# Performance work log

Hardware: AMD Instinct MI355X
Metric: run time of the kernel (lower is better)

Reference implementation:

```python
import jax, jax.numpy as jnp
import numpy as np
import math

B, Z, H, HID, T = 16384, 128, 512, 512, 32
MIN_BETA = 0.1


def setup_inputs() -> dict:
    key = jax.random.key(0)
    ks = jax.random.split(key, 8)
    # cosine beta schedule, matching torch init: (1-min)*cos(pi*(1-t)*0.5)**2 + min, t in linspace(1,0,T)
    ts = np.linspace(1.0, 0.0, T)
    beta = ((1.0 - MIN_BETA) * np.cos(math.pi * (1.0 - ts) * 0.5) ** 2 + MIN_BETA).astype(np.float32)
    s = 1.0 / np.sqrt(Z + H)
    return {
        "context_embedding": jax.random.normal(ks[0], (B, H), jnp.float32),
        "eps0": jax.random.normal(ks[1], (B, Z), jnp.float32),
        "eps": jax.random.normal(ks[2], (T, B, Z), jnp.float32),
        "beta_schedule": jnp.asarray(beta),
        "sigma0": jnp.ones((1,), jnp.float32),
        "W1": jax.random.normal(ks[3], (Z + H, HID), jnp.float32) * s,
        "b1": jnp.zeros((HID,), jnp.float32),
        "W2": jax.random.normal(ks[4], (HID, Z), jnp.float32) * (1.0 / np.sqrt(HID)),
        "b2": jnp.zeros((Z,), jnp.float32),
        "t_emb": jax.random.normal(ks[5], (T, HID), jnp.float32) * 0.02,
        "target_mu": jax.random.normal(ks[6], (B, Z), jnp.float32),
    }


def _normal_log_prob(x, mu, sigma):
    # elementwise Normal(mu, sigma).log_prob(x)
    half_log_2pi = 0.5 * jnp.log(2.0 * jnp.pi)
    return -0.5 * jnp.square((x - mu) / sigma) - jnp.log(sigma) - half_log_2pi


def reference(context_embedding, eps0, eps, beta_schedule, sigma0, W1, b1, W2, b2, t_emb, target_mu):
    num_steps = beta_schedule.shape[0]
    delta_t = 1.0 / num_steps
    sig0 = sigma0[0]

    # prior sample z_0 ~ N(0, sigma0)
    z0 = sig0 * eps0  # [B, Z]

    # backward kernel at loop index i uses beta_schedule[i-1]; i=0 wraps to beta_schedule[-1]
    beta_bwd = jnp.roll(beta_schedule, 1)

    def control(z, te):
        hid = jax.nn.relu(jnp.concatenate([z, context_embedding], axis=-1) @ W1 + b1 + te)
        return hid @ W2 + b2  # [B, Z]

    def step(carry, xs):
        z_prev, log_w = carry
        beta_f, beta_b, eps_t, te = xs
        u = control(z_prev, te)
        # forward kernel
        mu_f = z_prev + (beta_f * z_prev + u) * delta_t
        sig_f = jnp.sqrt(2.0 * beta_f * delta_t) * sig0
        z_next = mu_f + sig_f * eps_t  # rsample
        # backward kernel (evaluated at z_next)
        mu_b = z_next - beta_b * z_next * delta_t
        sig_b = jnp.sqrt(2.0 * beta_b * delta_t) * sig0
        log_w = log_w + _normal_log_prob(z_prev, mu_b, sig_b) - _normal_log_prob(z_next, mu_f, sig_f)
        return (z_next, log_w), None

    init = (z0, jnp.zeros_like(z0))
    (z_T, log_w), _ = jax.lax.scan(step, init, (beta_schedule, beta_bwd, eps, t_emb))

    # terminal + prior correction: p_z_T = N(target_mu, 1), p_z_0 = N(0, sigma0)
    log_w = log_w + _normal_log_prob(z_T, target_mu, 1.0) - _normal_log_prob(z0, 0.0, sig0)
    return jnp.sum(jnp.mean(log_w, axis=0))
```

## Files before the change

kernel.cpp:

```cpp
#include <hip/hip_runtime.h>
#include <hip/hip_bf16.h>

#define NB 16384
#define NZ 128
#define NH 512
#define NHID 512
#define NT 32

typedef __attribute__((ext_vector_type(8))) short short8;
typedef __attribute__((ext_vector_type(4))) short short4v;
typedef __attribute__((ext_vector_type(4))) float f32x4;

__device__ __forceinline__ short f2bf(float x) {
    union { __hip_bfloat16 h; short s; } u; u.h = __float2bfloat16(x); return u.s;
}
__device__ __forceinline__ float bf2f(short s) {
    union { unsigned int u; float f; } v; v.u = ((unsigned int)(unsigned short)s) << 16; return v.f;
}

__global__ __launch_bounds__(64) void pack_weights(const float* __restrict__ W1,
                                                   const float* __restrict__ W2,
                                                   short* __restrict__ w1aT,
                                                   long* __restrict__ w2T8,
                                                   short* __restrict__ w1bT) {
    int f = blockIdx.x;
    int l = threadIdx.x;
    int quad = l >> 4, m = l & 15;
    if (f < 128) {
        int ht = f >> 2, kt = f & 3;
        short8 o;
#pragma unroll
        for (int j = 0; j < 8; ++j)
            o[j] = f2bf(W1[(size_t)(kt * 32 + quad * 8 + j) * NH + ht * 16 + m]);
        *(short8*)(w1aT + ((size_t)f * 64 + l) * 8) = o;
    } else if (f < 256) {
        int g = f - 128; int kt2 = g >> 3, jt = g & 7;
        float v[8];
#pragma unroll
        for (int j = 0; j < 8; ++j)
            v[j] = W2[(size_t)(kt2 * 32 + quad * 8 + j) * NZ + jt * 16 + m];
        int lo = __builtin_amdgcn_cvt_pk_fp8_f32(v[0], v[1], 0, false);
        lo = __builtin_amdgcn_cvt_pk_fp8_f32(v[2], v[3], lo, true);
        int hi = __builtin_amdgcn_cvt_pk_fp8_f32(v[4], v[5], 0, false);
        hi = __builtin_amdgcn_cvt_pk_fp8_f32(v[6], v[7], hi, true);
        long pv = ((long)(unsigned int)hi << 32) | (unsigned int)lo;
        w2T8[(size_t)g * 64 + l] = pv;
    } else {
        int g = f - 256; int ht = g >> 4, kt = g & 15;
        short8 o;
#pragma unroll
        for (int j = 0; j < 8; ++j)
            o[j] = f2bf(W1[(size_t)(128 + kt * 32 + quad * 8 + j) * NH + ht * 16 + m]);
        *(short8*)(w1bT + ((size_t)g * 64 + l) * 8) = o;
    }
}

__global__ __launch_bounds__(512, 2) void diffusion_main(
    const float* __restrict__ eps0, const float* __restrict__ eps,
    const float* __restrict__ beta, const float* __restrict__ sigma0,
    const float* __restrict__ ctx, const float* __restrict__ b1,
    const float* __restrict__ b2, const float* __restrict__ t_emb,
    const float* __restrict__ target_mu,
    const short* __restrict__ w1aT, const short* __restrict__ w1bT,
    const long* __restrict__ w2T8, float* __restrict__ out)
{
    __shared__ alignas(16) char lds[50176];
    char* zu = lds;
    char* hidb = lds + 16384;
    float* scb = (float*)(lds + 49152);
    const int w = threadIdx.x >> 6;
    const int lane = threadIdx.x & 63;
    const int quad = lane >> 4;
    const int m = lane & 15;
    const int swz = m & 7;
    const int sw = swz << 1;
    const int rowbase = blockIdx.x * 64;
    const int ers = w >> 1;
    const int ek0 = (w & 1) << 1;
    const int erow = rowbase + ers * 16 + m;
    const float dt = 1.0f / 32.0f;
    const float s0 = sigma0[0];
    const float logs0 = logf(s0);
    const f32x4 zero = {0.f, 0.f, 0.f, 0.f};

    const int zu_base = m * 256 + ((quad ^ swz) << 4);
    const int hw_base = m * 512 + ((((quad ^ sw)) << 2) ^ (w << 6));
    const int hr_base = m * 512 + (((quad << 1) ^ sw) << 2);
    const int ubw_off = m * 256 + ((((w << 1) + (quad >> 1)) ^ swz) << 4) + ((quad & 1) << 3);

    if (threadIdx.x < 32) {
        int t = threadIdx.x;
        float bfv = beta[t];
        float bbv = beta[(t + 31) & 31];
        float sf = sqrtf(2.f * bfv * dt) * s0;
        float sb = sqrtf(2.f * bbv * dt) * s0;
        scb[t * 8 + 0] = bfv;
        scb[t * 8 + 1] = sf;
        scb[t * 8 + 2] = 1.f / sb;
        scb[t * 8 + 3] = 0.5f * (logf(bfv) - logf(bbv));
        scb[t * 8 + 4] = 1.f - bbv * dt;
    }

    f32x4 pacc[4][4];
#pragma unroll
    for (int c = 0; c < 4; ++c)
#pragma unroll
        for (int rs = 0; rs < 4; ++rs) pacc[c][rs] = zero;
#pragma unroll 4
    for (int kt = 0; kt < 16; ++kt) {
        short8 cf[4];
#pragma unroll
        for (int rs = 0; rs < 4; ++rs) {
            const float* cp = ctx + (size_t)(rowbase + rs * 16 + m) * NH + kt * 32 + quad * 8;
            f32x4 a = *(const f32x4*)cp;
            f32x4 b = *(const f32x4*)(cp + 4);
            short8 tt;
#pragma unroll
            for (int j = 0; j < 4; ++j) { tt[j] = f2bf(a[j]); tt[4 + j] = f2bf(b[j]); }
            cf[rs] = tt;
        }
#pragma unroll
        for (int c = 0; c < 4; ++c) {
            short8 af = *(const short8*)(w1bT + ((size_t)((w * 4 + c) * 16 + kt) * 64 + lane) * 8);
#pragma unroll
            for (int rs = 0; rs < 4; ++rs)
                pacc[c][rs] = __builtin_amdgcn_mfma_f32_16x16x32_bf16(af, cf[rs], pacc[c][rs], 0, 0, 0);
        }
    }
    short4v cbr[4][4];
#pragma unroll
    for (int c = 0; c < 4; ++c) {
        f32x4 bv = *(const f32x4*)(b1 + (w * 4 + c) * 16 + quad * 4);
#pragma unroll
        for (int rs = 0; rs < 4; ++rs) {
            short4v o;
#pragma unroll
            for (int i = 0; i < 4; ++i) o[i] = f2bf(pacc[c][rs][i] + bv[i]);
            cbr[c][rs] = o;
        }
    }
    f32x4 b2r = *(const f32x4*)(b2 + w * 16 + quad * 4);

    short8 wf1[4][4];
#pragma unroll
    for (int c = 0; c < 4; ++c)
#pragma unroll
        for (int kt = 0; kt < 4; ++kt)
            wf1[c][kt] = *(const short8*)(w1aT + ((size_t)((w * 4 + c) * 4 + kt) * 64 + lane) * 8);
    long wf2[16];
#pragma unroll
    for (int kt2 = 0; kt2 < 16; ++kt2)
        wf2[kt2] = w2T8[(size_t)(kt2 * 8 + w) * 64 + lane];

    float zr[2][8];
    float part = 0.f;
#pragma unroll
    for (int kk = 0; kk < 2; ++kk) {
        int kt = ek0 + kk;
        const float* ep = eps0 + (size_t)erow * NZ + kt * 32 + quad * 8;
        f32x4 a = *(const f32x4*)ep;
        f32x4 b = *(const f32x4*)(ep + 4);
        short8 zbw;
#pragma unroll
        for (int j = 0; j < 4; ++j) {
            zr[kk][j] = s0 * a[j]; zr[kk][4 + j] = s0 * b[j];
            zbw[j] = f2bf(zr[kk][j]); zbw[4 + j] = f2bf(zr[kk][4 + j]);
        }
        *(short8*)(zu + ers * 4096 + (zu_base ^ (kt << 6))) = zbw;
    }
    __syncthreads();

#pragma unroll 1
    for (int t = 0; t < NT; ++t) {
#pragma unroll
        for (int cc = 0; cc < 2; ++cc) {
            f32x4 g1[2][4];
#pragma unroll
            for (int c2 = 0; c2 < 2; ++c2)
#pragma unroll
                for (int rs = 0; rs < 4; ++rs) g1[c2][rs] = zero;
#pragma unroll
            for (int kt = 0; kt < 4; ++kt) {
                short8 zb[4];
#pragma unroll
                for (int rs = 0; rs < 4; ++rs)
                    zb[rs] = *(const short8*)(zu + rs * 4096 + (zu_base ^ (kt << 6)));
#pragma unroll
                for (int c2 = 0; c2 < 2; ++c2)
#pragma unroll
                    for (int rs = 0; rs < 4; ++rs)
                        g1[c2][rs] = __builtin_amdgcn_mfma_f32_16x16x32_bf16(
                            wf1[cc * 2 + c2][kt], zb[rs], g1[c2][rs], 0, 0, 0);
            }
#pragma unroll
            for (int c2 = 0; c2 < 2; ++c2) {
                int c = cc * 2 + c2;
                f32x4 te = *(const f32x4*)(t_emb + (size_t)t * NHID + (w * 4 + c) * 16 + quad * 4);
#pragma unroll
                for (int rs = 0; rs < 4; ++rs) {
                    float p0 = fmaxf(g1[c2][rs][0] + bf2f(cbr[c][rs][0]) + te[0], 0.f);
                    float p1 = fmaxf(g1[c2][rs][1] + bf2f(cbr[c][rs][1]) + te[1], 0.f);
                    float p2 = fmaxf(g1[c2][rs][2] + bf2f(cbr[c][rs][2]) + te[2], 0.f);
                    float p3 = fmaxf(g1[c2][rs][3] + bf2f(cbr[c][rs][3]) + te[3], 0.f);
                    int pk = __builtin_amdgcn_cvt_pk_fp8_f32(p0, p1, 0, false);
                    pk = __builtin_amdgcn_cvt_pk_fp8_f32(p2, p3, pk, true);
                    *(int*)(hidb + rs * 8192 + (hw_base ^ (c << 4))) = pk;
                }
            }
        }
        __syncthreads();

        f32x4 ef[2][2];
        {
            const float* ept = eps + (size_t)t * NB * NZ + (size_t)erow * NZ;
#pragma unroll
            for (int kk = 0; kk < 2; ++kk) {
                ef[kk][0] = *(const f32x4*)(ept + (ek0 + kk) * 32 + quad * 8);
                ef[kk][1] = *(const f32x4*)(ept + (ek0 + kk) * 32 + quad * 8 + 4);
            }
        }

        f32x4 ua[4];
#pragma unroll
        for (int rs = 0; rs < 4; ++rs) ua[rs] = zero;
#pragma unroll
        for (int kt2 = 0; kt2 < 16; ++kt2) {
            long wfr = wf2[kt2];
#pragma unroll
            for (int rs = 0; rs < 4; ++rs) {
                long hf = *(const long*)(hidb + rs * 8192 + (hr_base ^ (kt2 << 5)));
                ua[rs] = __builtin_amdgcn_mfma_f32_16x16x32_fp8_fp8(wfr, hf, ua[rs], 0, 0, 0);
            }
        }
#pragma unroll
        for (int rs = 0; rs < 4; ++rs) {
            short4v o;
#pragma unroll
            for (int i = 0; i < 4; ++i) o[i] = f2bf(ua[rs][i] + b2r[i]);
            *(short4v*)(zu + rs * 4096 + ubw_off) = o;
        }
        __builtin_amdgcn_s_waitcnt(0xC07F);
        __builtin_amdgcn_s_barrier();

        f32x4 sca = *(const f32x4*)(scb + t * 8);
        float c1mb = scb[t * 8 + 4];
#pragma unroll
        for (int kk = 0; kk < 2; ++kk) {
            int kt = ek0 + kk;
            char* gaddr = zu + ers * 4096 + (zu_base ^ (kt << 6));
            short8 uv = *(const short8*)gaddr;
            float ee[8];
#pragma unroll
            for (int j = 0; j < 4; ++j) { ee[j] = ef[kk][0][j]; ee[4 + j] = ef[kk][1][j]; }
            short8 zbw;
#pragma unroll
            for (int j = 0; j < 8; ++j) {
                float z = zr[kk][j];
                float e = ee[j];
                float uu = bf2f(uv[j]);
                float mu_f = z + (sca[0] * z + uu) * dt;
                float zn = mu_f + sca[1] * e;
                float d = (z - zn * c1mb) * sca[2];
                part += -0.5f * d * d + 0.5f * e * e + sca[3];
                zr[kk][j] = zn;
                zbw[j] = f2bf(zn);
            }
            *(short8*)gaddr = zbw;
        }
        __syncthreads();
    }

#pragma unroll
    for (int kk = 0; kk < 2; ++kk) {
        int kt = ek0 + kk;
        const float* ep = eps0 + (size_t)erow * NZ + kt * 32 + quad * 8;
        const float* tp = target_mu + (size_t)erow * NZ + kt * 32 + quad * 8;
        f32x4 a = *(const f32x4*)ep;
        f32x4 b = *(const f32x4*)(ep + 4);
        f32x4 ta = *(const f32x4*)tp;
        f32x4 tb = *(const f32x4*)(tp + 4);
#pragma unroll
        for (int j = 0; j < 4; ++j) {
            float d0 = zr[kk][j] - ta[j];
            float d1 = zr[kk][4 + j] - tb[j];
            part += -0.5f * d0 * d0 + 0.5f * a[j] * a[j] + logs0;
            part += -0.5f * d1 * d1 + 0.5f * b[j] * b[j] + logs0;
        }
    }
#pragma unroll
    for (int off = 32; off >= 1; off >>= 1) part += __shfl_xor(part, off, 64);
    if (lane == 0) atomicAdd(out, part * (1.0f / NB));
}

extern "C" void kernel_launch(void* const* d_in, const int* in_sizes, int n_in,
                              void* d_out, int out_size, void* d_ws, size_t ws_size,
                              hipStream_t stream) {
    const float* ctx  = (const float*)d_in[0];
    const float* eps0 = (const float*)d_in[1];
    const float* eps  = (const float*)d_in[2];
    const float* beta = (const float*)d_in[3];
    const float* sig0 = (const float*)d_in[4];
    const float* W1   = (const float*)d_in[5];
    const float* b1   = (const float*)d_in[6];
    const float* W2   = (const float*)d_in[7];
    const float* b2   = (const float*)d_in[8];
    const float* temb = (const float*)d_in[9];
    const float* tmu  = (const float*)d_in[10];
    float* out = (float*)d_out;

    char* ws = (char*)d_ws;
    short* w1aT = (short*)ws;
    long*  w2T8 = (long*)(ws + 131072);
    short* w1bT = (short*)(ws + 196608);

    hipMemsetAsync(d_out, 0, sizeof(float), stream);
    pack_weights<<<768, 64, 0, stream>>>(W1, W2, w1aT, w2T8, w1bT);
    diffusion_main<<<256, 512, 0, stream>>>(eps0, eps, beta, sig0, ctx, b1, b2,
                                            temb, tmu, w1aT, w1bT, w2T8, out);
}
```

Measured before the change: 560.7 us.

## Halve rows per block to 32 and double grid for higher occupancy

Each block now handles 32 batch rows instead of 64, halving LDS use, accumulator registers and per-wave row tiles, while the grid doubles to 512 blocks and launch bounds target 4 blocks per CU. The aim is to fill all CUs, which 256 blocks may not do on MI355X, and to hide latency with more resident waves. In exchange, each block repeats its weight-fragment loads into registers over half as many rows, and there is less MFMA work per barrier.

```diff
diff --git a/kernel.cpp b/kernel.cpp
--- a/kernel.cpp
+++ b/kernel.cpp
@@ -55,7 +55,7 @@
     }
 }
 
-__global__ __launch_bounds__(512, 2) void diffusion_main(
+__global__ __launch_bounds__(512, 4) void diffusion_main(
     const float* __restrict__ eps0, const float* __restrict__ eps,
     const float* __restrict__ beta, const float* __restrict__ sigma0,
     const float* __restrict__ ctx, const float* __restrict__ b1,
@@ -64,19 +64,19 @@
     const short* __restrict__ w1aT, const short* __restrict__ w1bT,
     const long* __restrict__ w2T8, float* __restrict__ out)
 {
-    __shared__ alignas(16) char lds[50176];
+    __shared__ alignas(16) char lds[25600];
     char* zu = lds;
-    char* hidb = lds + 16384;
-    float* scb = (float*)(lds + 49152);
+    char* hidb = lds + 8192;
+    float* scb = (float*)(lds + 24576);
     const int w = threadIdx.x >> 6;
     const int lane = threadIdx.x & 63;
     const int quad = lane >> 4;
     const int m = lane & 15;
     const int swz = m & 7;
     const int sw = swz << 1;
-    const int rowbase = blockIdx.x * 64;
-    const int ers = w >> 1;
-    const int ek0 = (w & 1) << 1;
+    const int rowbase = blockIdx.x * 32;
+    const int ers = w >> 2;
+    const int ekt = w & 3;
     const int erow = rowbase + ers * 16 + m;
     const float dt = 1.0f / 32.0f;
     const float s0 = sigma0[0];
@@ -101,16 +101,16 @@
         scb[t * 8 + 4] = 1.f - bbv * dt;
     }
 
-    f32x4 pacc[4][4];
+    f32x4 pacc[4][2];
 #pragma unroll
     for (int c = 0; c < 4; ++c)
 #pragma unroll
-        for (int rs = 0; rs < 4; ++rs) pacc[c][rs] = zero;
+        for (int rs = 0; rs < 2; ++rs) pacc[c][rs] = zero;
 #pragma unroll 4
     for (int kt = 0; kt < 16; ++kt) {
-        short8 cf[4];
-#pragma unroll
-        for (int rs = 0; rs < 4; ++rs) {
+        short8 cf[2];
+#pragma unroll
+        for (int rs = 0; rs < 2; ++rs) {
             const float* cp = ctx + (size_t)(rowbase + rs * 16 + m) * NH + kt * 32 + quad * 8;
             f32x4 a = *(const f32x4*)cp;
             f32x4 b = *(const f32x4*)(cp + 4);
@@ -123,16 +123,16 @@
         for (int c = 0; c < 4; ++c) {
             short8 af = *(const short8*)(w1bT + ((size_t)((w * 4 + c) * 16 + kt) * 64 + lane) * 8);
 #pragma unroll
-            for (int rs = 0; rs < 4; ++rs)
+            for (int rs = 0; rs < 2; ++rs)
                 pacc[c][rs] = __builtin_amdgcn_mfma_f32_16x16x32_bf16(af, cf[rs], pacc[c][rs], 0, 0, 0);
         }
     }
-    short4v cbr[4][4];
+    short4v cbr[4][2];
 #pragma unroll
     for (int c = 0; c < 4; ++c) {
         f32x4 bv = *(const f32x4*)(b1 + (w * 4 + c) * 16 + quad * 4);
 #pragma unroll
-        for (int rs = 0; rs < 4; ++rs) {
+        for (int rs = 0; rs < 2; ++rs) {
             short4v o;
 #pragma unroll
             for (int i = 0; i < 4; ++i) o[i] = f2bf(pacc[c][rs][i] + bv[i]);
@@ -152,21 +152,19 @@
     for (int kt2 = 0; kt2 < 16; ++kt2)
         wf2[kt2] = w2T8[(size_t)(kt2 * 8 + w) * 64 + lane];
 
-    float zr[2][8];
+    float zr[8];
     float part = 0.f;
-#pragma unroll
-    for (int kk = 0; kk < 2; ++kk) {
-        int kt = ek0 + kk;
-        const float* ep = eps0 + (size_t)erow * NZ + kt * 32 + quad * 8;
+    {
+        const float* ep = eps0 + (size_t)erow * NZ + ekt * 32 + quad * 8;
         f32x4 a = *(const f32x4*)ep;
         f32x4 b = *(const f32x4*)(ep + 4);
         short8 zbw;
 #pragma unroll
         for (int j = 0; j < 4; ++j) {
-            zr[kk][j] = s0 * a[j]; zr[kk][4 + j] = s0 * b[j];
-            zbw[j] = f2bf(zr[kk][j]); zbw[4 + j] = f2bf(zr[kk][4 + j]);
-        }
-        *(short8*)(zu + ers * 4096 + (zu_base ^ (kt << 6))) = zbw;
+            zr[j] = s0 * a[j]; zr[4 + j] = s0 * b[j];
+            zbw[j] = f2bf(zr[j]); zbw[4 + j] = f2bf(zr[4 + j]);
+        }
+        *(short8*)(zu + ers * 4096 + (zu_base ^ (ekt << 6))) = zbw;
     }
     __syncthreads();
 
@@ -174,21 +172,21 @@
     for (int t = 0; t < NT; ++t) {
 #pragma unroll
         for (int cc = 0; cc < 2; ++cc) {
-            f32x4 g1[2][4];
+            f32x4 g1[2][2];
 #pragma unroll
             for (int c2 = 0; c2 < 2; ++c2)
 #pragma unroll
-                for (int rs = 0; rs < 4; ++rs) g1[c2][rs] = zero;
+                for (int rs = 0; rs < 2; ++rs) g1[c2][rs] = zero;
 #pragma unroll
             for (int kt = 0; kt < 4; ++kt) {
-                short8 zb[4];
-#pragma unroll
-                for (int rs = 0; rs < 4; ++rs)
+                short8 zb[2];
+#pragma unroll
+                for (int rs = 0; rs < 2; ++rs)
                     zb[rs] = *(const short8*)(zu + rs * 4096 + (zu_base ^ (kt << 6)));
 #pragma unroll
                 for (int c2 = 0; c2 < 2; ++c2)
 #pragma unroll
-                    for (int rs = 0; rs < 4; ++rs)
+                    for (int rs = 0; rs < 2; ++rs)
                         g1[c2][rs] = __builtin_amdgcn_mfma_f32_16x16x32_bf16(
                             wf1[cc * 2 + c2][kt], zb[rs], g1[c2][rs], 0, 0, 0);
             }
@@ -197,7 +195,7 @@
                 int c = cc * 2 + c2;
                 f32x4 te = *(const f32x4*)(t_emb + (size_t)t * NHID + (w * 4 + c) * 16 + quad * 4);
 #pragma unroll
-                for (int rs = 0; rs < 4; ++rs) {
+                for (int rs = 0; rs < 2; ++rs) {
                     float p0 = fmaxf(g1[c2][rs][0] + bf2f(cbr[c][rs][0]) + te[0], 0.f);
                     float p1 = fmaxf(g1[c2][rs][1] + bf2f(cbr[c][rs][1]) + te[1], 0.f);
                     float p2 = fmaxf(g1[c2][rs][2] + bf2f(cbr[c][rs][2]) + te[2], 0.f);
@@ -210,30 +208,27 @@
         }
         __syncthreads();
 
-        f32x4 ef[2][2];
+        f32x4 ef[2];
         {
             const float* ept = eps + (size_t)t * NB * NZ + (size_t)erow * NZ;
-#pragma unroll
-            for (int kk = 0; kk < 2; ++kk) {
-                ef[kk][0] = *(const f32x4*)(ept + (ek0 + kk) * 32 + quad * 8);
-                ef[kk][1] = *(const f32x4*)(ept + (ek0 + kk) * 32 + quad * 8 + 4);
-            }
-        }
-
-        f32x4 ua[4];
-#pragma unroll
-        for (int rs = 0; rs < 4; ++rs) ua[rs] = zero;
+            ef[0] = *(const f32x4*)(ept + ekt * 32 + quad * 8);
+            ef[1] = *(const f32x4*)(ept + ekt * 32 + quad * 8 + 4);
+        }
+
+        f32x4 ua[2];
+#pragma unroll
+        for (int rs = 0; rs < 2; ++rs) ua[rs] = zero;
 #pragma unroll
         for (int kt2 = 0; kt2 < 16; ++kt2) {
             long wfr = wf2[kt2];
 #pragma unroll
-            for (int rs = 0; rs < 4; ++rs) {
+            for (int rs = 0; rs < 2; ++rs) {
                 long hf = *(const long*)(hidb + rs * 8192 + (hr_base ^ (kt2 << 5)));
                 ua[rs] = __builtin_amdgcn_mfma_f32_16x16x32_fp8_fp8(wfr, hf, ua[rs], 0, 0, 0);
             }
         }
 #pragma unroll
-        for (int rs = 0; rs < 4; ++rs) {
+        for (int rs = 0; rs < 2; ++rs) {
             short4v o;
 #pragma unroll
             for (int i = 0; i < 4; ++i) o[i] = f2bf(ua[rs][i] + b2r[i]);
@@ -244,25 +239,23 @@
 
         f32x4 sca = *(const f32x4*)(scb + t * 8);
         float c1mb = scb[t * 8 + 4];
-#pragma unroll
-        for (int kk = 0; kk < 2; ++kk) {
-            int kt = ek0 + kk;
-            char* gaddr = zu + ers * 4096 + (zu_base ^ (kt << 6));
+        {
+            char* gaddr = zu + ers * 4096 + (zu_base ^ (ekt << 6));
             short8 uv = *(const short8*)gaddr;
             float ee[8];
 #pragma unroll
-            for (int j = 0; j < 4; ++j) { ee[j] = ef[kk][0][j]; ee[4 + j] = ef[kk][1][j]; }
+            for (int j = 0; j < 4; ++j) { ee[j] = ef[0][j]; ee[4 + j] = ef[1][j]; }
             short8 zbw;
 #pragma unroll
             for (int j = 0; j < 8; ++j) {
-                float z = zr[kk][j];
+                float z = zr[j];
                 float e = ee[j];
                 float uu = bf2f(uv[j]);
                 float mu_f = z + (sca[0] * z + uu) * dt;
                 float zn = mu_f + sca[1] * e;
                 float d = (z - zn * c1mb) * sca[2];
                 part += -0.5f * d * d + 0.5f * e * e + sca[3];
-                zr[kk][j] = zn;
+                zr[j] = zn;
                 zbw[j] = f2bf(zn);
             }
             *(short8*)gaddr = zbw;
@@ -270,19 +263,17 @@
         __syncthreads();
     }
 
-#pragma unroll
-    for (int kk = 0; kk < 2; ++kk) {
-        int kt = ek0 + kk;
-        const float* ep = eps0 + (size_t)erow * NZ + kt * 32 + quad * 8;
-        const float* tp = target_mu + (size_t)erow * NZ + kt * 32 + quad * 8;
+    {
+        const float* ep = eps0 + (size_t)erow * NZ + ekt * 32 + quad * 8;
+        const float* tp = target_mu + (size_t)erow * NZ + ekt * 32 + quad * 8;
         f32x4 a = *(const f32x4*)ep;
         f32x4 b = *(const f32x4*)(ep + 4);
         f32x4 ta = *(const f32x4*)tp;
         f32x4 tb = *(const f32x4*)(tp + 4);
 #pragma unroll
         for (int j = 0; j < 4; ++j) {
-            float d0 = zr[kk][j] - ta[j];
-            float d1 = zr[kk][4 + j] - tb[j];
+            float d0 = zr[j] - ta[j];
+            float d1 = zr[4 + j] - tb[j];
             part += -0.5f * d0 * d0 + 0.5f * a[j] * a[j] + logs0;
             part += -0.5f * d1 * d1 + 0.5f * b[j] * b[j] + logs0;
         }
@@ -315,6 +306,6 @@
 
     hipMemsetAsync(d_out, 0, sizeof(float), stream);
     pack_weights<<<768, 64, 0, stream>>>(W1, W2, w1aT, w2T8, w1bT);
-    diffusion_main<<<256, 512, 0, stream>>>(eps0, eps, beta, sig0, ctx, b1, b2,
+    diffusion_main<<<512, 512, 0, stream>>>(eps0, eps, beta, sig0, ctx, b1, b2,
                                             temb, tmu, w1aT, w1bT, w2T8, out);
 }
```

Result: slower. 979.7 us (+74.7%).

## Keep z state in MFMA output layout to drop a barrier per step

Applied to the files above, without the earlier changes.

The per-row z state now lives in the same lane/column layout as the second GEMM's accumulator. The drift update runs directly on the MFMA outputs instead of writing u to LDS and reading it back, which removes one LDS round-trip and one block barrier per timestep. The hidden-activation LDS layout is re-swizzled so the second GEMM can fetch two fp8 K-slices with one 16-byte read. The eps load is hoisted to the top of each step to overlap with the first GEMM. The cost is a new swizzle scheme that must stay conflict-free and correct.

```diff
diff --git a/kernel.cpp b/kernel.cpp
--- a/kernel.cpp
+++ b/kernel.cpp
@@ -10,6 +10,7 @@
 typedef __attribute__((ext_vector_type(8))) short short8;
 typedef __attribute__((ext_vector_type(4))) short short4v;
 typedef __attribute__((ext_vector_type(4))) float f32x4;
+typedef __attribute__((ext_vector_type(2))) long long2v;
 
 __device__ __forceinline__ short f2bf(float x) {
     union { __hip_bfloat16 h; short s; } u; u.h = __float2bfloat16(x); return u.s;
@@ -73,20 +74,18 @@
     const int quad = lane >> 4;
     const int m = lane & 15;
     const int swz = m & 7;
-    const int sw = swz << 1;
     const int rowbase = blockIdx.x * 64;
-    const int ers = w >> 1;
-    const int ek0 = (w & 1) << 1;
-    const int erow = rowbase + ers * 16 + m;
+    const int jcol = w * 16 + quad * 4;
     const float dt = 1.0f / 32.0f;
     const float s0 = sigma0[0];
     const float logs0 = logf(s0);
     const f32x4 zero = {0.f, 0.f, 0.f, 0.f};
 
     const int zu_base = m * 256 + ((quad ^ swz) << 4);
-    const int hw_base = m * 512 + ((((quad ^ sw)) << 2) ^ (w << 6));
-    const int hr_base = m * 512 + (((quad << 1) ^ sw) << 2);
-    const int ubw_off = m * 256 + ((((w << 1) + (quad >> 1)) ^ swz) << 4) + ((quad & 1) << 3);
+    const int zw_off  = m * 256 + ((((w << 1) + (quad >> 1)) ^ swz) << 4)
+                      + ((quad & 1) << 3);
+    const int hw_base = m * 512 + ((quad & 1) << 2);
+    const int hr_base = m * 512;
 
     if (threadIdx.x < 32) {
         int t = threadIdx.x;
@@ -139,7 +138,7 @@
             cbr[c][rs] = o;
         }
     }
-    f32x4 b2r = *(const f32x4*)(b2 + w * 16 + quad * 4);
+    f32x4 b2r = *(const f32x4*)(b2 + jcol);
 
     short8 wf1[4][4];
 #pragma unroll
@@ -152,26 +151,29 @@
     for (int kt2 = 0; kt2 < 16; ++kt2)
         wf2[kt2] = w2T8[(size_t)(kt2 * 8 + w) * 64 + lane];
 
-    float zr[2][8];
+    float zr[4][4];
     float part = 0.f;
 #pragma unroll
-    for (int kk = 0; kk < 2; ++kk) {
-        int kt = ek0 + kk;
-        const float* ep = eps0 + (size_t)erow * NZ + kt * 32 + quad * 8;
-        f32x4 a = *(const f32x4*)ep;
-        f32x4 b = *(const f32x4*)(ep + 4);
-        short8 zbw;
-#pragma unroll
-        for (int j = 0; j < 4; ++j) {
-            zr[kk][j] = s0 * a[j]; zr[kk][4 + j] = s0 * b[j];
-            zbw[j] = f2bf(zr[kk][j]); zbw[4 + j] = f2bf(zr[kk][4 + j]);
-        }
-        *(short8*)(zu + ers * 4096 + (zu_base ^ (kt << 6))) = zbw;
-    }
-    __syncthreads();
+    for (int rs = 0; rs < 4; ++rs) {
+        f32x4 e = *(const f32x4*)(eps0 + (size_t)(rowbase + rs * 16 + m) * NZ + jcol);
+        short4v zb;
+#pragma unroll
+        for (int i = 0; i < 4; ++i) { zr[rs][i] = s0 * e[i]; zb[i] = f2bf(zr[rs][i]); }
+        *(short4v*)(zu + rs * 4096 + zw_off) = zb;
+    }
+    __builtin_amdgcn_s_waitcnt(0xC07F);
+    __builtin_amdgcn_s_barrier();
 
 #pragma unroll 1
     for (int t = 0; t < NT; ++t) {
+        f32x4 ef[4];
+        {
+            const float* ept = eps + (size_t)t * NB * NZ + (size_t)rowbase * NZ + jcol;
+#pragma unroll
+            for (int rs = 0; rs < 4; ++rs)
+                ef[rs] = *(const f32x4*)(ept + (size_t)(rs * 16 + m) * NZ);
+        }
+
 #pragma unroll
         for (int cc = 0; cc < 2; ++cc) {
             f32x4 g1[2][4];
@@ -195,6 +197,8 @@
 #pragma unroll
             for (int c2 = 0; c2 < 2; ++c2) {
                 int c = cc * 2 + c2;
+                int Gc = (((w * 4 + ((c & 1) << 1) + (quad >> 1)) ^ m) << 4)
+                       + (((c >> 1) & 1) << 3);
                 f32x4 te = *(const f32x4*)(t_emb + (size_t)t * NHID + (w * 4 + c) * 16 + quad * 4);
 #pragma unroll
                 for (int rs = 0; rs < 4; ++rs) {
@@ -204,87 +208,63 @@
                     float p3 = fmaxf(g1[c2][rs][3] + bf2f(cbr[c][rs][3]) + te[3], 0.f);
                     int pk = __builtin_amdgcn_cvt_pk_fp8_f32(p0, p1, 0, false);
                     pk = __builtin_amdgcn_cvt_pk_fp8_f32(p2, p3, pk, true);
-                    *(int*)(hidb + rs * 8192 + (hw_base ^ (c << 4))) = pk;
+                    *(int*)(hidb + rs * 8192 + hw_base + Gc) = pk;
                 }
             }
         }
-        __syncthreads();
-
-        f32x4 ef[2][2];
-        {
-            const float* ept = eps + (size_t)t * NB * NZ + (size_t)erow * NZ;
-#pragma unroll
-            for (int kk = 0; kk < 2; ++kk) {
-                ef[kk][0] = *(const f32x4*)(ept + (ek0 + kk) * 32 + quad * 8);
-                ef[kk][1] = *(const f32x4*)(ept + (ek0 + kk) * 32 + quad * 8 + 4);
-            }
-        }
-
-        f32x4 ua[4];
-#pragma unroll
-        for (int rs = 0; rs < 4; ++rs) ua[rs] = zero;
-#pragma unroll
-        for (int kt2 = 0; kt2 < 16; ++kt2) {
-            long wfr = wf2[kt2];
-#pragma unroll
-            for (int rs = 0; rs < 4; ++rs) {
-                long hf = *(const long*)(hidb + rs * 8192 + (hr_base ^ (kt2 << 5)));
-                ua[rs] = __builtin_amdgcn_mfma_f32_16x16x32_fp8_fp8(wfr, hf, ua[rs], 0, 0, 0);
-            }
-        }
-#pragma unroll
-        for (int rs = 0; rs < 4; ++rs) {
-            short4v o;
-#pragma unroll
-            for (int i = 0; i < 4; ++i) o[i] = f2bf(ua[rs][i] + b2r[i]);
-            *(short4v*)(zu + rs * 4096 + ubw_off) = o;
-        }
         __builtin_amdgcn_s_waitcnt(0xC07F);
         __builtin_amdgcn_s_barrier();
 
         f32x4 sca = *(const f32x4*)(scb + t * 8);
         float c1mb = scb[t * 8 + 4];
-#pragma unroll
-        for (int kk = 0; kk < 2; ++kk) {
-            int kt = ek0 + kk;
-            char* gaddr = zu + ers * 4096 + (zu_base ^ (kt << 6));
-            short8 uv = *(const short8*)gaddr;
-            float ee[8];
-#pragma unroll
-            for (int j = 0; j < 4; ++j) { ee[j] = ef[kk][0][j]; ee[4 + j] = ef[kk][1][j]; }
-            short8 zbw;
-#pragma unroll
-            for (int j = 0; j < 8; ++j) {
-                float z = zr[kk][j];
-                float e = ee[j];
-                float uu = bf2f(uv[j]);
+
+        f32x4 ua[4];
+#pragma unroll
+        for (int rs = 0; rs < 4; ++rs) ua[rs] = zero;
+#pragma unroll
+        for (int kp = 0; kp < 8; ++kp) {
+            long wlo = wf2[kp * 2];
+            long whi = wf2[kp * 2 + 1];
+            int go = ((kp * 4 + quad) ^ m) << 4;
+#pragma unroll
+            for (int rs = 0; rs < 4; ++rs) {
+                long2v h2 = *(const long2v*)(hidb + rs * 8192 + hr_base + go);
+                ua[rs] = __builtin_amdgcn_mfma_f32_16x16x32_fp8_fp8(wlo, h2[0], ua[rs], 0, 0, 0);
+                ua[rs] = __builtin_amdgcn_mfma_f32_16x16x32_fp8_fp8(whi, h2[1], ua[rs], 0, 0, 0);
+            }
+        }
+
+#pragma unroll
+        for (int rs = 0; rs < 4; ++rs) {
+            short4v zb;
+#pragma unroll
+            for (int i = 0; i < 4; ++i) {
+                float z = zr[rs][i];
+                float e = ef[rs][i];
+                float uu = ua[rs][i] + b2r[i];
                 float mu_f = z + (sca[0] * z + uu) * dt;
                 float zn = mu_f + sca[1] * e;
                 float d = (z - zn * c1mb) * sca[2];
                 part += -0.5f * d * d + 0.5f * e * e + sca[3];
-                zr[kk][j] = zn;
-                zbw[j] = f2bf(zn);
+                zr[rs][i] = zn;
+                zb[i] = f2bf(zn);
             }
-            *(short8*)gaddr = zbw;
-        }
-        __syncthreads();
-    }
-
-#pragma unroll
-    for (int kk = 0; kk < 2; ++kk) {
-        int kt = ek0 + kk;
-        const float* ep = eps0 + (size_t)erow * NZ + kt * 32 + quad * 8;
-        const float* tp = target_mu + (size_t)erow * NZ + kt * 32 + quad * 8;
+            *(short4v*)(zu + rs * 4096 + zw_off) = zb;
+        }
+        __builtin_amdgcn_s_waitcnt(0xC07F);
+        __builtin_amdgcn_s_barrier();
+    }
+
+#pragma unroll
+    for (int rs = 0; rs < 4; ++rs) {
+        const float* ep = eps0 + (size_t)(rowbase + rs * 16 + m) * NZ + jcol;
+        const float* tp = target_mu + (size_t)(rowbase + rs * 16 + m) * NZ + jcol;
         f32x4 a = *(const f32x4*)ep;
-        f32x4 b = *(const f32x4*)(ep + 4);
         f32x4 ta = *(const f32x4*)tp;
-        f32x4 tb = *(const f32x4*)(tp + 4);
-#pragma unroll
-        for (int j = 0; j < 4; ++j) {
-            float d0 = zr[kk][j] - ta[j];
-            float d1 = zr[kk][4 + j] - tb[j];
-            part += -0.5f * d0 * d0 + 0.5f * a[j] * a[j] + logs0;
-            part += -0.5f * d1 * d1 + 0.5f * b[j] * b[j] + logs0;
+#pragma unroll
+        for (int i = 0; i < 4; ++i) {
+            float d0 = zr[rs][i] - ta[i];
+            part += -0.5f * d0 * d0 + 0.5f * a[i] * a[i] + logs0;
         }
     }
 #pragma unroll
```

Measured after the change: 687.5 us. +22.6%, slower.
